# Kernel optimization log

Hardware: AMD Instinct MI355X
Metric: run time of the kernel (lower is better)

## Reference

```python
import jax, jax.numpy as jnp
import numpy as np
import math

B, T, D = 2, 4096, 2048
H, d_head, C = 16, 128, 64


def binarize(x):
    # sign to {-1,+1} with straight-through estimator (identity gradient)
    s = jnp.where(x >= 0, jnp.ones_like(x), -jnp.ones_like(x))
    return x + jax.lax.stop_gradient(s - x)


def setup_inputs() -> dict:
    key = jax.random.key(0)
    ks = jax.random.split(key, 5)
    w_std = 1.0 / math.sqrt(D)
    return {
        "x": jax.random.normal(ks[0], (B, T, D), dtype=jnp.float32),
        "Wq": jax.random.normal(ks[1], (D, D), dtype=jnp.float32) * w_std,
        "Wk": jax.random.normal(ks[2], (D, D), dtype=jnp.float32) * w_std,
        "Wv": jax.random.normal(ks[3], (D, D), dtype=jnp.float32) * w_std,
        "Wo": jax.random.normal(ks[4], (D, D), dtype=jnp.float32) * w_std,
    }


def reference(x, Wq, Wk, Wv, Wo):
    Bx, Tx, Dx = x.shape
    scale = 1.0 / math.sqrt(d_head)
    # projections (torch Linear: y = x @ W.T), split heads -> [B,H,T,d]
    q = (x @ Wq.T).reshape(Bx, Tx, H, d_head).transpose(0, 2, 1, 3) * scale
    k = binarize((x @ Wk.T).reshape(Bx, Tx, H, d_head).transpose(0, 2, 1, 3))
    v = binarize((x @ Wv.T).reshape(Bx, Tx, H, d_head).transpose(0, 2, 1, 3))
    N = Tx // C  # T chosen divisible by chunk_size
    qc = q.reshape(Bx, H, N, C, d_head)
    kc = k.reshape(Bx, H, N, C, d_head)
    vc = v.reshape(Bx, H, N, C, d_head)
    # intra-chunk causal attention
    mask = jnp.tril(jnp.ones((C, C), dtype=x.dtype))
    intra_scores = jnp.einsum('bhnid,bhnjd->bhnij', qc, kc) * mask
    intra = jnp.einsum('bhnij,bhnjd->bhnid', intra_scores, vc)
    # cross-chunk: exclusive prefix sum of per-chunk k^T v outer products
    chunk_kv = jnp.einsum('bhnci,bhncj->bhnij', kc, vc)  # [B,H,N,d,d]
    cs = jnp.cumsum(chunk_kv, axis=2)
    prefix = cs - chunk_kv  # exclusive cumsum
    cross = jnp.einsum('bhncd,bhnde->bhnce', qc, prefix)
    output = (intra + cross).reshape(Bx, H, Tx, d_head)
    out = output.transpose(0, 2, 1, 3).reshape(Bx, Tx, Dx) @ Wo.T
    final_state = cs[:, :, -1]  # [B,H,d,d]
    return out, final_state
```

## Files before the change

kernel.cpp:

```cpp
#include <hip/hip_runtime.h>
#include <stdint.h>

typedef __attribute__((ext_vector_type(8))) short short8;
typedef __attribute__((ext_vector_type(4))) float f32x4;
typedef unsigned short u16;
typedef unsigned long long u64;

__device__ __forceinline__ u16 f2bf(float f) {
  uint32_t u = __builtin_bit_cast(uint32_t, f);
  u = (u + 0x7FFFu + ((u >> 16) & 1u)) >> 16;
  return (u16)u;
}
__device__ __forceinline__ float bf2f(u16 h) {
  uint32_t u = ((uint32_t)h) << 16;
  return __builtin_bit_cast(float, u);
}
__device__ __forceinline__ void lds16(const u16* g, u16* l) {
  __builtin_amdgcn_global_load_lds(
      (const __attribute__((address_space(1))) void*)g,
      (__attribute__((address_space(3))) void*)l, 16, 0, 0);
}
__device__ __forceinline__ int sw256(int i) { return i ^ (((i >> 7) & 7) << 3); }
__device__ __forceinline__ int sw128(int i) { return i ^ (((i >> 6) & 7) << 3); }
__device__ __forceinline__ int swzA64(int i) { return i ^ (((i >> 6) & 7) << 3); }
__device__ __forceinline__ int swzA32(int i) { return i ^ (((i >> 6) & 3) << 3); }

#define SB0() __builtin_amdgcn_sched_barrier(0)
#define BAR() __builtin_amdgcn_s_barrier()
#define LGKM0() do { asm volatile("s_waitcnt lgkmcnt(0)" ::: "memory"); SB0(); } while (0)
#define VM(n) asm volatile("s_waitcnt vmcnt(" #n ")" ::: "memory")
#define VMNOP do {} while (0)

__global__ __launch_bounds__(256) void split_all(
    const float* __restrict__ x,  const float* __restrict__ Wq,
    const float* __restrict__ Wk, const float* __restrict__ Wv,
    const float* __restrict__ Wo,
    u16* __restrict__ xh, u16* __restrict__ xl,
    u16* __restrict__ qh, u16* __restrict__ kh, u16* __restrict__ kl,
    u16* __restrict__ vh, u16* __restrict__ vl, u16* __restrict__ oh)
{
  const int bid = blockIdx.x, t = threadIdx.x;
  if (bid < 2048) {
    for (int i = bid * 256 + t; i < 2097152; i += 2048 * 256) {
      const float4* s = (const float4*)x + 2 * (size_t)i;
      float4 a = s[0], b = s[1];
      float v[8] = {a.x, a.y, a.z, a.w, b.x, b.y, b.z, b.w};
      short8 hi, lo;
#pragma unroll
      for (int j = 0; j < 8; j++) {
        u16 h = f2bf(v[j]);
        hi[j] = (short)h;
        lo[j] = (short)f2bf(v[j] - bf2f(h));
      }
      ((short8*)xh)[i] = hi;
      ((short8*)xl)[i] = lo;
    }
  } else {
    const int seg = (bid - 2048) >> 9;
    const int sb  = (bid - 2048) & 511;
    const float* W = seg == 0 ? Wq : seg == 1 ? Wk : seg == 2 ? Wv : Wo;
    u16* H = seg == 0 ? qh : seg == 1 ? kh : seg == 2 ? vh : oh;
    u16* L = seg == 1 ? kl : seg == 2 ? vl : nullptr;
    for (int i = sb * 256 + t; i < 524288; i += 512 * 256) {
      const float4* s = (const float4*)W + 2 * (size_t)i;
      float4 a = s[0], b = s[1];
      float v[8] = {a.x, a.y, a.z, a.w, b.x, b.y, b.z, b.w};
      short8 hi, lo;
#pragma unroll
      for (int j = 0; j < 8; j++) {
        u16 h = f2bf(v[j]);
        hi[j] = (short)h;
        lo[j] = (short)f2bf(v[j] - bf2f(h));
      }
      ((short8*)H)[i] = hi;
      if (L) ((short8*)L)[i] = lo;
    }
  }
}

template<int SPLIT, int EPI, int NTN>
__global__ __launch_bounds__(512, 2) void gemm8p(
    const u16* __restrict__ Ahi, const u16* __restrict__ Alo,
    const u16* __restrict__ Bhi, const u16* __restrict__ Blo,
    u16* __restrict__ outb, float* __restrict__ outf,
    u64* __restrict__ kpk_p, u64* __restrict__ vpk_p,
    int Mdim, int Ndim, int Kdim)
{
  constexpr int BK   = (SPLIT > 1) ? 32 : 64;
  constexpr int TILE = 256 * BK;
  constexpr int NMAT = (SPLIT > 1) ? 4 : 2;
  constexpr int AOFF_H = 0;
  constexpr int AOFF_L = (SPLIT > 1) ? TILE : 0;
  constexpr int BOFF_H = (SPLIT > 1) ? 2*TILE : TILE;
  constexpr int BOFF_L = (SPLIT > 1) ? 3*TILE : 0;
  __shared__ __align__(16) u16 smem[2 * NMAT * TILE];

  const int t = threadIdx.x, l = t & 63;
  const int w = t >> 6;
  const int wm = w >> 2, wn = w & 3;
  const int fr = l & 15, fs = l >> 4;
  const int sb = (blockIdx.x & 7) * (4 * NTN) + (blockIdx.x >> 3);
  const int m0 = (sb / NTN) * 256, n0 = (sb % NTN) * 256;
  const int NT = Kdim / BK;

  auto ST = [&](const u16* src, int g0, int moff, int kt, int r) {
    if (kt >= NT) return;
    const int bufb = (kt & 1) * NMAT * TILE;
    int d = r * 4096 + t * 8;
    int row, scol;
    if constexpr (SPLIT == 1) { row = d >> 6; scol = ((d >> 3) & 7) ^ (row & 7); }
    else                      { row = d >> 5; scol = ((d >> 3) & 3) ^ ((row >> 1) & 3); }
    lds16(src + (size_t)(g0 + row) * Kdim + kt * BK + scol * 8,
          smem + bufb + moff + d);
  };

  f32x4 acc[8][4] = {};

#define SWZ(i) ((BK == 64) ? swzA64(i) : swzA32(i))
  auto RD8 = [&](short8* dst, int bufb, int off) {
#pragma unroll
    for (int fm = 0; fm < 8; fm++) {
      int ia = (wm*128 + fm*16 + fr)*BK + fs*8;
      dst[fm] = *(const short8*)(smem + bufb + off + SWZ(ia));
    }
  };
  auto RD4 = [&](short8* dst, int bufb, int off) {
#pragma unroll
    for (int fn = 0; fn < 4; fn++) {
      int ib = (wn*64 + fn*16 + fr)*BK + fs*8;
      dst[fn] = *(const short8*)(smem + bufb + off + SWZ(ib));
    }
  };
  auto RDQ = [&](short8* dst, int bufb, int q) {
#pragma unroll
    for (int i = 0; i < 2; i++)
#pragma unroll
      for (int ks = 0; ks < 2; ks++) {
        int ia = (wm*128 + (2*q+i)*16 + fr)*64 + ks*32 + fs*8;
        dst[i*2+ks] = *(const short8*)(smem + bufb + AOFF_H + swzA64(ia));
      }
  };
  auto RDB8 = [&](short8* dst, int bufb) {
#pragma unroll
    for (int fn = 0; fn < 4; fn++)
#pragma unroll
      for (int ks = 0; ks < 2; ks++) {
        int ib = (wn*64 + fn*16 + fr)*64 + ks*32 + fs*8;
        dst[fn*2+ks] = *(const short8*)(smem + bufb + BOFF_H + swzA64(ib));
      }
  };

#define PASS32(RA, RB) do {                                                    \
  __builtin_amdgcn_s_setprio(1);                                               \
  _Pragma("unroll") for (int fm_ = 0; fm_ < 8; fm_++)                          \
    _Pragma("unroll") for (int fn_ = 0; fn_ < 4; fn_++)                        \
      acc[fm_][fn_] = __builtin_amdgcn_mfma_f32_16x16x32_bf16(                 \
          (RA)[fm_], (RB)[fn_], acc[fm_][fn_], 0, 0, 0);                       \
  __builtin_amdgcn_s_setprio(0);                                               \
  SB0();                                                                       \
} while (0)

#define PASS16(Q, AQ, BB) do {                                                 \
  __builtin_amdgcn_s_setprio(1);                                               \
  _Pragma("unroll") for (int i_ = 0; i_ < 2; i_++)                             \
    _Pragma("unroll") for (int fn_ = 0; fn_ < 4; fn_++)                        \
      _Pragma("unroll") for (int ks_ = 0; ks_ < 2; ks_++)                      \
        acc[2*(Q)+i_][fn_] = __builtin_amdgcn_mfma_f32_16x16x32_bf16(          \
            (AQ)[i_*2+ks_], (BB)[fn_*2+ks_], acc[2*(Q)+i_][fn_], 0, 0, 0);     \
  __builtin_amdgcn_s_setprio(0);                                               \
  SB0();                                                                       \
} while (0)

#define T3BODY(T, W0, W1, W2) {                                                \
  const int bufb = ((T) & 1) * NMAT * TILE;                                    \
  short8 xah[8], xbh[4], xbl[4], xal[8];                                       \
  RD8(xah, bufb, AOFF_H); RD4(xbh, bufb, BOFF_H);                              \
  ST(Ahi, m0, AOFF_H, (T)+1, 0); ST(Ahi, m0, AOFF_H, (T)+1, 1);                \
  ST(Bhi, n0, BOFF_H, (T)+1, 0); ST(Bhi, n0, BOFF_H, (T)+1, 1);                \
  W0; BAR(); LGKM0(); PASS32(xah, xbh); BAR();                                 \
  RD4(xbl, bufb, BOFF_L);                                                      \
  ST(Blo, n0, BOFF_L, (T)+1, 0); ST(Blo, n0, BOFF_L, (T)+1, 1);                \
  W1; BAR(); LGKM0(); PASS32(xah, xbl); BAR();                                 \
  RD8(xal, bufb, AOFF_L);                                                      \
  ST(Alo, m0, AOFF_L, (T)+1, 0); ST(Alo, m0, AOFF_L, (T)+1, 1);                \
  W2; BAR(); LGKM0(); PASS32(xal, xbh); BAR();                                 \
}

#define T1BODY(T, W1, W3) {                                                    \
  const int bufb = ((T) & 1) * NMAT * TILE;                                    \
  short8 bb[8], aq[4];                                                         \
  RDB8(bb, bufb); RDQ(aq, bufb, 0);                                            \
  ST(Bhi, n0, BOFF_H, (T)+1, 0); ST(Bhi, n0, BOFF_H, (T)+1, 1);                \
  BAR(); LGKM0(); PASS16(0, aq, bb); BAR();                                    \
  RDQ(aq, bufb, 1);                                                            \
  ST(Bhi, n0, BOFF_H, (T)+1, 2); ST(Bhi, n0, BOFF_H, (T)+1, 3);                \
  W1; BAR(); LGKM0(); PASS16(1, aq, bb); BAR();                                \
  RDQ(aq, bufb, 2);                                                            \
  ST(Ahi, m0, AOFF_H, (T)+1, 0); ST(Ahi, m0, AOFF_H, (T)+1, 2);                \
  BAR(); LGKM0(); PASS16(2, aq, bb); BAR();                                    \
  RDQ(aq, bufb, 3);                                                            \
  ST(Ahi, m0, AOFF_H, (T)+1, 1); ST(Ahi, m0, AOFF_H, (T)+1, 3);                \
  W3; BAR(); LGKM0(); PASS16(3, aq, bb); BAR();                                \
}

  if constexpr (SPLIT > 1) {
    ST(Ahi, m0, AOFF_H, 0, 0); ST(Ahi, m0, AOFF_H, 0, 1);
    ST(Bhi, n0, BOFF_H, 0, 0); ST(Bhi, n0, BOFF_H, 0, 1);
    ST(Blo, n0, BOFF_L, 0, 0); ST(Blo, n0, BOFF_L, 0, 1);
    ST(Alo, m0, AOFF_L, 0, 0); ST(Alo, m0, AOFF_L, 0, 1);
    VM(4); BAR();
    for (int T = 0; T < NT - 1; T++) T3BODY(T, VM(6), VM(6), VM(4))
    T3BODY(NT - 1, VM(2), VM(0), VMNOP)
  } else {
    ST(Bhi, n0, BOFF_H, 0, 0); ST(Bhi, n0, BOFF_H, 0, 1);
    ST(Bhi, n0, BOFF_H, 0, 2); ST(Bhi, n0, BOFF_H, 0, 3);
    ST(Ahi, m0, AOFF_H, 0, 0); ST(Ahi, m0, AOFF_H, 0, 2);
    ST(Ahi, m0, AOFF_H, 0, 1); ST(Ahi, m0, AOFF_H, 0, 3);
    VM(2); BAR();
    for (int T = 0; T < NT - 1; T++) T1BODY(T, VM(4), VM(2))
    T1BODY(NT - 1, VM(0), VMNOP)
  }
#undef SWZ
#undef T3BODY
#undef T1BODY
#undef PASS32
#undef PASS16

  if constexpr (EPI == 1) {
#pragma unroll
    for (int q = 0; q < 2; q++) {
#pragma unroll
      for (int fn = 0; fn < 4; fn++) {
        u64 bal[4][4];
#pragma unroll
        for (int j = 0; j < 4; j++)
#pragma unroll
          for (int r = 0; r < 4; r++)
            bal[j][r] = __ballot(acc[4*q + j][fn][r] < 0.f);
        if (l < 16) {
          u64 wq = 0;
#pragma unroll
          for (int j = 0; j < 4; j++)
#pragma unroll
            for (int r = 0; r < 4; r++) {
              u64 x = (bal[j][r] >> l) & 0x0001000100010001ULL;
              u64 y = (x & 1) | ((x >> 12) & 0x10) |
                      ((x >> 24) & 0x100) | ((x >> 36) & 0x1000);
              wq |= y << (j*16 + r);
            }
          int gmc = m0 + wm*128 + q*64;
          int gn  = n0 + wn*64 + fn*16 + l;
          int b = gmc >> 12, n = (gmc & 4095) >> 6;
          int kv = gn >> 11, h = (gn >> 7) & 15, dd = gn & 127;
          u64* dst = kv ? vpk_p : kpk_p;
          dst[((size_t)((b*16 + h)*64 + n))*128 + dd] = wq;
        }
      }
    }
  } else {
    const float qscale = 0.08838834764831843f;
#pragma unroll
    for (int fm = 0; fm < 8; fm++)
#pragma unroll
      for (int fn = 0; fn < 4; fn++)
#pragma unroll
        for (int r = 0; r < 4; r++) {
          int gm = m0 + wm*128 + fm*16 + fs*4 + r;
          int gn = n0 + wn*64 + fn*16 + fr;
          float val = acc[fm][fn][r];
          if constexpr (EPI == 2) {
            outf[(size_t)gm * Ndim + gn] = val;
          } else {
            int b = gm >> 12, tt = gm & 4095, h = gn >> 7, dd = gn & 127;
            size_t idx = (((size_t)(b*16 + h))*4096 + tt)*128 + dd;
            outb[idx] = f2bf(val * qscale);
          }
        }
  }
}

__global__ __launch_bounds__(256) void scan_kernel(
    const u64* __restrict__ kp, const u64* __restrict__ vp,
    short* __restrict__ pfx8, float* __restrict__ fstate)
{
  __shared__ float xch[256];
  const int t = threadIdx.x;
  const int bh = blockIdx.x >> 6, ep = blockIdx.x & 63;
  const int e = ep * 2 + (t >> 7), d = t & 127;
  const size_t base = (size_t)bh * 64 * 128;
  int s = 0;
  for (int n = 0; n < 64; n++) {
    if ((n & 7) == 0)
      pfx8[((size_t)(bh*8 + (n>>3))*128 + e)*128 + d] = (short)s;
    u64 kw = kp[base + (size_t)n*128 + d];
    u64 vw = vp[base + (size_t)n*128 + e];
    s += 64 - 2*__popcll(kw ^ vw);
  }
  xch[t] = (float)s;
  __syncthreads();
  if (t < 128) {
    float2 p;
    p.x = xch[t];
    p.y = xch[t + 128];
    *(float2*)&fstate[((size_t)bh*128 + t)*128 + ep*2] = p;
  }
}

__global__ __launch_bounds__(256) void fused_attn(
    const u16* __restrict__ q,
    const u64* __restrict__ kp, const u64* __restrict__ vp,
    const short* __restrict__ pfx8, u16* __restrict__ att)
{
  __shared__ __align__(16) u16 smem[16384];
  u16* sP1 = smem;
  u16* sP2 = smem + 8192;
  u16* sS  = sP1 + 4096;

  const int t = threadIdx.x, l = t & 63, w = t >> 6;
  const int blk = blockIdx.x, bh = blk >> 6, n = blk & 63;
  const int b = bh >> 4, hh = bh & 15;
  const int fr = l & 15, fs = l >> 4;
  const size_t qbase = (((size_t)bh * 4096) + n * 64) * 128;
  const size_t pbase = (size_t)bh * 64 * 128;

  short8 qv[4];
#pragma unroll
  for (int kk = 0; kk < 4; kk++)
    qv[kk] = *(const short8*)(q + qbase + (size_t)(w*16 + fr)*128 + kk*32 + fs*8);

  {
    const u64* krow = kp + pbase + (size_t)n*128;
    int d = (t & 63) * 2, c0 = (t >> 6) * 16;
    u64 w0 = krow[d], w1 = krow[d+1];
#pragma unroll
    for (int i = 0; i < 16; i++) {
      int c = c0 + i;
      uint32_t b0 = ((w0 >> c) & 1ull) ? 0xBF80u : 0x3F80u;
      uint32_t b1 = ((w1 >> c) & 1ull) ? 0xBF80u : 0x3F80u;
      *(uint32_t*)(sP1 + sw256(c*128 + d)) = b0 | (b1 << 16);
    }
  }
  {
    int d = t >> 1, ch = (t & 1) * 32;
    u64 wv = vp[pbase + (size_t)n*128 + d];
#pragma unroll
    for (int c = 0; c < 32; c += 2) {
      uint32_t b0 = ((wv >> (ch + c)) & 1ull)     ? 0xBF80u : 0x3F80u;
      uint32_t b1 = ((wv >> (ch + c + 1)) & 1ull) ? 0xBF80u : 0x3F80u;
      int li = d*64 + ch + c;
      *(uint32_t*)(sP2 + sw128(li)) = b0 | (b1 << 16);
    }
  }
  __syncthreads();

  f32x4 accS[4] = {};
#pragma unroll
  for (int kk = 0; kk < 4; kk++) {
#pragma unroll
    for (int fn = 0; fn < 4; fn++) {
      int lb = (fn*16 + fr)*128 + kk*32 + fs*8;
      short8 bb = *(const short8*)(sP1 + sw256(lb));
      accS[fn] = __builtin_amdgcn_mfma_f32_16x16x32_bf16(qv[kk], bb, accS[fn], 0, 0, 0);
    }
  }
  __syncthreads();
#pragma unroll
  for (int fn = 0; fn < 4; fn++)
#pragma unroll
    for (int r = 0; r < 4; r++) {
      int i = w*16 + fs*4 + r, j = fn*16 + fr;
      float v = (j <= i) ? accS[fn][r] : 0.f;
      sS[sw128(i*64 + j)] = f2bf(v);
    }
  __syncthreads();

  f32x4 accI[8] = {};
#pragma unroll
  for (int kk = 0; kk < 2; kk++) {
    int la = (w*16 + fr)*64 + kk*32 + fs*8;
    short8 a = *(const short8*)(sS + sw128(la));
#pragma unroll
    for (int fn = 0; fn < 8; fn++) {
      int lb = (fn*16 + fr)*64 + kk*32 + fs*8;
      short8 bb = *(const short8*)(sP2 + sw128(lb));
      accI[fn] = __builtin_amdgcn_mfma_f32_16x16x32_bf16(a, bb, accI[fn], 0, 0, 0);
    }
  }
  __syncthreads();

  const int m0 = n & ~7, cnt = n & 7;
  for (int hf = 0; hf < 2; hf++) {
#pragma unroll
    for (int p = 0; p < 4; p++) {
      int erow = p*16 + (t>>4);
      int e = hf*64 + erow;
      const short* ps = pfx8 + ((size_t)(bh*8 + (n>>3))*128 + e)*128 + (t&15)*8;
      short8 pv = *(const short8*)ps;
      int accj[8];
#pragma unroll
      for (int j = 0; j < 8; j++) accj[j] = pv[j];
      for (int m = 0; m < cnt; m++) {
        u64 vw = vp[pbase + (size_t)(m0+m)*128 + e];
#pragma unroll
        for (int j = 0; j < 8; j++) {
          u64 kw = kp[pbase + (size_t)(m0+m)*128 + (t&15)*8 + j];
          accj[j] += 64 - 2*__popcll(kw ^ vw);
        }
      }
      short8 hi, lo;
#pragma unroll
      for (int j = 0; j < 8; j++) {
        hi[j] = (short)f2bf((float)(accj[j] >> 5));
        lo[j] = (short)f2bf((float)(accj[j] & 31));
      }
      int pi = sw256(erow*128 + (t&15)*8);
      *(short8*)(sP1 + pi) = hi;
      *(short8*)(sP2 + pi) = lo;
    }
    __syncthreads();

    f32x4 acch[4] = {}, accl[4] = {};
#pragma unroll
    for (int kk = 0; kk < 4; kk++) {
#pragma unroll
      for (int fn = 0; fn < 4; fn++) {
        int pb = sw256((fn*16 + fr)*128 + kk*32 + fs*8);
        acch[fn] = __builtin_amdgcn_mfma_f32_16x16x32_bf16(qv[kk], *(const short8*)(sP1 + pb), acch[fn], 0, 0, 0);
        accl[fn] = __builtin_amdgcn_mfma_f32_16x16x32_bf16(qv[kk], *(const short8*)(sP2 + pb), accl[fn], 0, 0, 0);
      }
    }
#pragma unroll
    for (int fn = 0; fn < 4; fn++)
#pragma unroll
      for (int r = 0; r < 4; r++) {
        int c = w*16 + fs*4 + r;
        int dcol = hf*64 + fn*16 + fr;
        float val = accI[hf*4+fn][r] + 32.f*acch[fn][r] + accl[fn][r];
        size_t idx = ((size_t)(b*4096 + n*64 + c))*2048 + hh*128 + dcol;
        att[idx] = f2bf(val);
      }
    __syncthreads();
  }
}

extern "C" void kernel_launch(void* const* d_in, const int* in_sizes, int n_in,
                              void* d_out, int out_size, void* d_ws, size_t ws_size,
                              hipStream_t stream) {
  (void)in_sizes; (void)n_in; (void)out_size; (void)ws_size;
  const float* x  = (const float*)d_in[0];
  const float* Wq = (const float*)d_in[1];
  const float* Wk = (const float*)d_in[2];
  const float* Wv = (const float*)d_in[3];
  const float* Wo = (const float*)d_in[4];
  float* out = (float*)d_out;
  float* fstate = out + (size_t)16777216;

  char* ws = (char*)d_ws;
  u16* x_hi = (u16*)(ws + 0);
  u16* x_lo = (u16*)(ws + 33554432);
  u16* qb   = (u16*)(ws + 67108864);
  u16* wq_h  = (u16*)(ws + 167772160);
  u16* wkv_h = (u16*)(ws + 176160768);
  u16* wkv_l = (u16*)(ws + 192937984);
  u16* wo_h  = (u16*)(ws + 209715200);
  u64* kpk = (u64*)(ws + 218103808);
  u64* vpk = (u64*)(ws + 220200960);
  u16* att    = x_hi;
  short* pfx8 = (short*)(ws + 134217728);

  split_all<<<4096, 256, 0, stream>>>(x, Wq, Wk, Wv, Wo,
                                      x_hi, x_lo, wq_h,
                                      wkv_h, wkv_l,
                                      wkv_h + 4194304, wkv_l + 4194304,
                                      wo_h);

  gemm8p<1,0,8><<<256, 512, 0, stream>>>(x_hi, nullptr, wq_h, nullptr, qb, nullptr,
                                         nullptr, nullptr, 8192, 2048, 2048);
  gemm8p<3,1,16><<<512, 512, 0, stream>>>(x_hi, x_lo, wkv_h, wkv_l, nullptr, nullptr,
                                          kpk, vpk, 8192, 4096, 2048);

  scan_kernel<<<2048, 256, 0, stream>>>(kpk, vpk, pfx8, fstate);
  fused_attn<<<2048, 256, 0, stream>>>(qb, kpk, vpk, pfx8, att);

  gemm8p<1,2,8><<<256, 512, 0, stream>>>(att, nullptr, wo_h, nullptr, nullptr, out,
                                         nullptr, nullptr, 8192, 2048, 2048);
}
```

Before: 639.3 us.

## Replace BK=64 quarter-pass pipeline with simple BK=32 double-buffered loop for single-split GEMM

For the non-split GEMM path, the K tile shrinks from 64 to 32 and the four-phase quarter-tile pipeline (RDQ/RDB8/PASS16, with staggered partial loads and vmcnt waits) is removed. It is replaced by a simple loop that reads the full A/B fragments, issues next-tile global-to-LDS loads, runs one full MFMA pass, then waits on all loads and barriers. This halves LDS usage for that path and simplifies scheduling, but it exposes load latency on every iteration (VM(0) before the barrier) and doubles the number of K iterations.

Result: no change. 649.2 us (+1.5%).

```diff
diff --git a/kernel.cpp b/kernel.cpp
--- a/kernel.cpp
+++ b/kernel.cpp
@@ -22,7 +22,6 @@
 }
 __device__ __forceinline__ int sw256(int i) { return i ^ (((i >> 7) & 7) << 3); }
 __device__ __forceinline__ int sw128(int i) { return i ^ (((i >> 6) & 7) << 3); }
-__device__ __forceinline__ int swzA64(int i) { return i ^ (((i >> 6) & 7) << 3); }
 __device__ __forceinline__ int swzA32(int i) { return i ^ (((i >> 6) & 3) << 3); }
 
 #define SB0() __builtin_amdgcn_sched_barrier(0)
@@ -86,7 +85,7 @@
     u64* __restrict__ kpk_p, u64* __restrict__ vpk_p,
     int Mdim, int Ndim, int Kdim)
 {
-  constexpr int BK   = (SPLIT > 1) ? 32 : 64;
+  constexpr int BK   = 32;
   constexpr int TILE = 256 * BK;
   constexpr int NMAT = (SPLIT > 1) ? 4 : 2;
   constexpr int AOFF_H = 0;
@@ -107,47 +106,26 @@
     if (kt >= NT) return;
     const int bufb = (kt & 1) * NMAT * TILE;
     int d = r * 4096 + t * 8;
-    int row, scol;
-    if constexpr (SPLIT == 1) { row = d >> 6; scol = ((d >> 3) & 7) ^ (row & 7); }
-    else                      { row = d >> 5; scol = ((d >> 3) & 3) ^ ((row >> 1) & 3); }
+    int row = d >> 5, scol = ((d >> 3) & 3) ^ ((row >> 1) & 3);
     lds16(src + (size_t)(g0 + row) * Kdim + kt * BK + scol * 8,
           smem + bufb + moff + d);
   };
 
   f32x4 acc[8][4] = {};
 
-#define SWZ(i) ((BK == 64) ? swzA64(i) : swzA32(i))
   auto RD8 = [&](short8* dst, int bufb, int off) {
 #pragma unroll
     for (int fm = 0; fm < 8; fm++) {
       int ia = (wm*128 + fm*16 + fr)*BK + fs*8;
-      dst[fm] = *(const short8*)(smem + bufb + off + SWZ(ia));
+      dst[fm] = *(const short8*)(smem + bufb + off + swzA32(ia));
     }
   };
   auto RD4 = [&](short8* dst, int bufb, int off) {
 #pragma unroll
     for (int fn = 0; fn < 4; fn++) {
       int ib = (wn*64 + fn*16 + fr)*BK + fs*8;
-      dst[fn] = *(const short8*)(smem + bufb + off + SWZ(ib));
-    }
-  };
-  auto RDQ = [&](short8* dst, int bufb, int q) {
-#pragma unroll
-    for (int i = 0; i < 2; i++)
-#pragma unroll
-      for (int ks = 0; ks < 2; ks++) {
-        int ia = (wm*128 + (2*q+i)*16 + fr)*64 + ks*32 + fs*8;
-        dst[i*2+ks] = *(const short8*)(smem + bufb + AOFF_H + swzA64(ia));
-      }
-  };
-  auto RDB8 = [&](short8* dst, int bufb) {
-#pragma unroll
-    for (int fn = 0; fn < 4; fn++)
-#pragma unroll
-      for (int ks = 0; ks < 2; ks++) {
-        int ib = (wn*64 + fn*16 + fr)*64 + ks*32 + fs*8;
-        dst[fn*2+ks] = *(const short8*)(smem + bufb + BOFF_H + swzA64(ib));
-      }
+      dst[fn] = *(const short8*)(smem + bufb + off + swzA32(ib));
+    }
   };
 
 #define PASS32(RA, RB) do {                                                    \
@@ -156,17 +134,6 @@
     _Pragma("unroll") for (int fn_ = 0; fn_ < 4; fn_++)                        \
       acc[fm_][fn_] = __builtin_amdgcn_mfma_f32_16x16x32_bf16(                 \
           (RA)[fm_], (RB)[fn_], acc[fm_][fn_], 0, 0, 0);                       \
-  __builtin_amdgcn_s_setprio(0);                                               \
-  SB0();                                                                       \
-} while (0)
-
-#define PASS16(Q, AQ, BB) do {                                                 \
-  __builtin_amdgcn_s_setprio(1);                                               \
-  _Pragma("unroll") for (int i_ = 0; i_ < 2; i_++)                             \
-    _Pragma("unroll") for (int fn_ = 0; fn_ < 4; fn_++)                        \
-      _Pragma("unroll") for (int ks_ = 0; ks_ < 2; ks_++)                      \
-        acc[2*(Q)+i_][fn_] = __builtin_amdgcn_mfma_f32_16x16x32_bf16(          \
-            (AQ)[i_*2+ks_], (BB)[fn_*2+ks_], acc[2*(Q)+i_][fn_], 0, 0, 0);     \
   __builtin_amdgcn_s_setprio(0);                                               \
   SB0();                                                                       \
 } while (0)
@@ -186,23 +153,6 @@
   W2; BAR(); LGKM0(); PASS32(xal, xbh); BAR();                                 \
 }
 
-#define T1BODY(T, W1, W3) {                                                    \
-  const int bufb = ((T) & 1) * NMAT * TILE;                                    \
-  short8 bb[8], aq[4];                                                         \
-  RDB8(bb, bufb); RDQ(aq, bufb, 0);                                            \
-  ST(Bhi, n0, BOFF_H, (T)+1, 0); ST(Bhi, n0, BOFF_H, (T)+1, 1);                \
-  BAR(); LGKM0(); PASS16(0, aq, bb); BAR();                                    \
-  RDQ(aq, bufb, 1);                                                            \
-  ST(Bhi, n0, BOFF_H, (T)+1, 2); ST(Bhi, n0, BOFF_H, (T)+1, 3);                \
-  W1; BAR(); LGKM0(); PASS16(1, aq, bb); BAR();                                \
-  RDQ(aq, bufb, 2);                                                            \
-  ST(Ahi, m0, AOFF_H, (T)+1, 0); ST(Ahi, m0, AOFF_H, (T)+1, 2);                \
-  BAR(); LGKM0(); PASS16(2, aq, bb); BAR();                                    \
-  RDQ(aq, bufb, 3);                                                            \
-  ST(Ahi, m0, AOFF_H, (T)+1, 1); ST(Ahi, m0, AOFF_H, (T)+1, 3);                \
-  W3; BAR(); LGKM0(); PASS16(3, aq, bb); BAR();                                \
-}
-
   if constexpr (SPLIT > 1) {
     ST(Ahi, m0, AOFF_H, 0, 0); ST(Ahi, m0, AOFF_H, 0, 1);
     ST(Bhi, n0, BOFF_H, 0, 0); ST(Bhi, n0, BOFF_H, 0, 1);
@@ -212,19 +162,24 @@
     for (int T = 0; T < NT - 1; T++) T3BODY(T, VM(6), VM(6), VM(4))
     T3BODY(NT - 1, VM(2), VM(0), VMNOP)
   } else {
+    ST(Ahi, m0, AOFF_H, 0, 0); ST(Ahi, m0, AOFF_H, 0, 1);
     ST(Bhi, n0, BOFF_H, 0, 0); ST(Bhi, n0, BOFF_H, 0, 1);
-    ST(Bhi, n0, BOFF_H, 0, 2); ST(Bhi, n0, BOFF_H, 0, 3);
-    ST(Ahi, m0, AOFF_H, 0, 0); ST(Ahi, m0, AOFF_H, 0, 2);
-    ST(Ahi, m0, AOFF_H, 0, 1); ST(Ahi, m0, AOFF_H, 0, 3);
-    VM(2); BAR();
-    for (int T = 0; T < NT - 1; T++) T1BODY(T, VM(4), VM(2))
-    T1BODY(NT - 1, VM(0), VMNOP)
-  }
-#undef SWZ
+    VM(0); BAR();
+    for (int T = 0; T < NT; T++) {
+      const int cb = (T & 1) * NMAT * TILE;
+      short8 a[8], bq[4];
+      RD8(a, cb, AOFF_H); RD4(bq, cb, BOFF_H);
+      SB0();
+      ST(Ahi, m0, AOFF_H, T+1, 0); ST(Ahi, m0, AOFF_H, T+1, 1);
+      ST(Bhi, n0, BOFF_H, T+1, 0); ST(Bhi, n0, BOFF_H, T+1, 1);
+      SB0();
+      LGKM0();
+      PASS32(a, bq);
+      VM(0); BAR();
+    }
+  }
 #undef T3BODY
-#undef T1BODY
 #undef PASS32
-#undef PASS16
 
   if constexpr (EPI == 1) {
 #pragma unroll
```
